# Kernel optimization log

Hardware: AMD Instinct MI355X
Metric: run time of the kernel (lower is better)

## Reference

```python
import jax, jax.numpy as jnp
import numpy as np

B, BS, M, D = 64, 8, 512, 256  # b = bs * neg_sample_num, neg_sample_num = 8
NEG_FILL = -1e10


def setup_inputs() -> dict:
    key = jax.random.key(0)
    ks = jax.random.split(key, 7)
    x = jax.random.normal(ks[0], (B, M, D), jnp.float32)
    y = jax.random.normal(ks[1], (BS, M, D), jnp.float32)
    mask_x = jax.random.randint(ks[2], (B, M), 0, 2).astype(bool).at[:, 0].set(True)
    mask_y = jax.random.randint(ks[3], (BS, M), 0, 2).astype(bool).at[:, 0].set(True)
    scale = 1.0 / np.sqrt(D)
    Wq = jax.random.normal(ks[4], (D, D), jnp.float32) * scale  # torch Linear weight [out,in]
    Wk = jax.random.normal(ks[5], (D, D), jnp.float32) * scale
    Wv = jax.random.normal(ks[6], (D, D), jnp.float32) * scale
    return {"x": x, "y": y, "mask_x": mask_x, "mask_y": mask_y, "Wq": Wq, "Wk": Wk, "Wv": Wv}


def reference(x, y, mask_x, mask_y, Wq, Wk, Wv):
    # Projections (torch Linear: x @ W.T, no bias)
    Qx, Kx, Vx = x @ Wq.T, x @ Wk.T, x @ Wv.T
    Qy, Ky, Vy = y @ Wq.T, y @ Wk.T, y @ Wv.T
    b, m, d = Qx.shape
    bs = Ky.shape[0]
    neg = b // bs  # neg_sample_num branch (bs != b)

    scores_x = jnp.einsum('bid,bjd->bij', Qx, Kx)   # [b,m,m]
    scores_y = jnp.einsum('bid,bjd->bij', Qy, Ky)   # [bs,m,m]
    # Q_x grouped as [bs, neg, m, d] then transposed to [neg, bs, m, d];
    # K_y is tiled over neg (pure broadcast), so contract directly against [bs,m,d].
    Qx_e = Qx.reshape(bs, neg, m, d).swapaxes(0, 1)  # [neg,bs,m,d]
    scores_xy = jnp.einsum('nsid,sjd->nsij', Qx_e, Ky)  # [neg,bs,m,m]

    mx = mask_x[:, :, None]  # [b,m,1]
    my = mask_y[:, :, None]  # [bs,m,1]
    scores_x = jnp.where(mx & mx.swapaxes(1, 2), scores_x, NEG_FILL)
    scores_y = jnp.where(my & my.swapaxes(1, 2), scores_y, NEG_FILL)

    mask_xy = mask_x.reshape(bs, neg, m, 1).swapaxes(0, 1) & mask_y[None, :, None, :]  # [neg,bs,m,m]
    scores_xy = jnp.where(mask_xy, scores_xy, NEG_FILL)

    # y_len[n, s] = sum(mask_y[s]) for every n (repeat/view/sum/transpose in torch)
    y_len = jnp.broadcast_to(jnp.sum(mask_y.astype(jnp.int32), axis=1)[None, :], (neg, bs))

    probs_x = jax.nn.softmax(scores_x, axis=-1)
    probs_y = jax.nn.softmax(scores_y, axis=-1)
    probs_xy = jax.nn.softmax(scores_xy, axis=-1)

    ctx_x = jnp.einsum('bij,bjd->bid', probs_x, Vx)
    ctx_y = jnp.einsum('bij,bjd->bid', probs_y, Vy)
    return (ctx_x, ctx_y, scores_x, scores_y, probs_xy, mask_xy, y_len)
```

## Files before the change

kernel.cpp:

```cpp
#include <hip/hip_runtime.h>
#include <cstdint>

#define NEG_FILL_F (-10000000000.0f)
constexpr int BB     = 64;
constexpr int BS_    = 8;
constexpr int MM     = 512;
constexpr int DD     = 256;
constexpr int ROWS_X = BB * MM;
constexpr int ROWS_Y = BS_ * MM;
constexpr int ROWS_ALL = ROWS_X + ROWS_Y;
constexpr int K3     = 768;

typedef __attribute__((ext_vector_type(8))) short short8;
typedef __attribute__((ext_vector_type(4))) float f32x4;

__device__ inline unsigned short rne_bf16(float f) {
    unsigned int u = __float_as_uint(f);
    u = (u + 0x7FFFu + ((u >> 16) & 1u)) >> 16;
    return (unsigned short)u;
}
__device__ inline float bf2f(unsigned short h) {
    return __uint_as_float(((unsigned int)h) << 16);
}

__device__ inline f32x4 mfma16(short8 a, short8 b, f32x4 c) {
    return __builtin_amdgcn_mfma_f32_16x16x32_bf16(a, b, c, 0, 0, 0);
}

__device__ inline void gld16(const unsigned short* g, unsigned short* l) {
    __builtin_amdgcn_global_load_lds(
        (const __attribute__((address_space(1))) unsigned int*)g,
        (__attribute__((address_space(3))) unsigned int*)l, 16, 0, 0);
}

template<int LDA, int LDB>
__device__ inline void mfma_tiles(const unsigned short (*Ab)[LDA],
                                  const unsigned short (*Bb)[LDB],
                                  int kk, int wrow, int wcol, int lid, int quad,
                                  f32x4 acc[4][4])
{
    short8 af[4], bfr[4];
    #pragma unroll
    for (int i = 0; i < 4; ++i)
        af[i] = *(const short8*)&Ab[wrow + i * 16 + lid][kk + quad * 8];
    #pragma unroll
    for (int j = 0; j < 4; ++j)
        bfr[j] = *(const short8*)&Bb[wcol + j * 16 + lid][kk + quad * 8];
    #pragma unroll
    for (int i = 0; i < 4; ++i)
        #pragma unroll
        for (int j = 0; j < 4; ++j)
            acc[i][j] = mfma16(af[i], bfr[j], acc[i][j]);
}

__device__ inline void stage768_async(unsigned short* dstbase,
                                      const unsigned short* __restrict__ src,
                                      int ck, int wave, int lane)
{
    #pragma unroll
    for (int s = 0; s < 6; ++s) {
        const int c   = s * 256 + wave * 64 + lane;
        const int row = c / 12;
        const int kc  = (c % 12) * 8;
        gld16(src + (size_t)row * K3 + ck * 96 + kc,
              dstbase + (size_t)(s * 256 + wave * 64) * 8);
    }
}

__device__ inline void stage_x96(unsigned short (*dst)[96],
                                 const float* __restrict__ src,
                                 int ck, int t)
{
    #pragma unroll
    for (int s = 0; s < 4; ++s) {
        const int c   = s * 256 + t;
        const int row = c >> 3;
        const int q4  = (c & 7) * 4;
        float4 v = *(const float4*)(src + (size_t)row * DD + ck * 32 + q4);
        const float fv[4] = {v.x, v.y, v.z, v.w};
        unsigned short o[12];
        #pragma unroll
        for (int e = 0; e < 4; ++e) {
            unsigned short h = rne_bf16(fv[e]);
            unsigned short l = rne_bf16(fv[e] - bf2f(h));
            o[e*3+0] = h; o[e*3+1] = l; o[e*3+2] = h;
        }
        ushort4* p = (ushort4*)&dst[row][q4 * 3];
        p[0] = make_ushort4(o[0], o[1], o[2],  o[3]);
        p[1] = make_ushort4(o[4], o[5], o[6],  o[7]);
        p[2] = make_ushort4(o[8], o[9], o[10], o[11]);
    }
}

__global__ __launch_bounds__(256) void convw_kernel(
    const float* __restrict__ Wq, const float* __restrict__ Wk,
    const float* __restrict__ Wv, unsigned short* __restrict__ Wb)
{
    const int g  = blockIdx.x * 256 + threadIdx.x;
    const int e  = g * 8;
    const int zi = e >> 16;
    const int off = e & 65535;
    const float* W = (zi == 0) ? Wq : (zi == 1 ? Wk : Wv);
    float4 v0 = *(const float4*)(W + off);
    float4 v1 = *(const float4*)(W + off + 4);
    const float fv[8] = {v0.x, v0.y, v0.z, v0.w, v1.x, v1.y, v1.z, v1.w};
    unsigned short o[24];
    #pragma unroll
    for (int i = 0; i < 8; ++i) {
        unsigned short h = rne_bf16(fv[i]);
        unsigned short l = rne_bf16(fv[i] - bf2f(h));
        o[i*3+0] = h; o[i*3+1] = h; o[i*3+2] = l;
    }
    unsigned short* dst = Wb + (size_t)zi * 196608 + (size_t)off * 3;
    #pragma unroll
    for (int s = 0; s < 3; ++s) {
        short8 v;
        #pragma unroll
        for (int e2 = 0; e2 < 8; ++e2) v[e2] = (short)o[s*8+e2];
        *(short8*)(dst + s * 8) = v;
    }
}

__global__ __launch_bounds__(256) void proj_kernel(
    const float* __restrict__ x, const float* __restrict__ y,
    const unsigned short* __restrict__ Wb,
    unsigned short* __restrict__ Qa, unsigned short* __restrict__ Kb,
    unsigned short* __restrict__ Vt)
{
    const int z    = blockIdx.z;
    const int row0 = blockIdx.x * 128;
    const int col0 = blockIdx.y * 128;
    const float* A = (row0 < ROWS_X) ? (x + (size_t)row0 * DD)
                                     : (y + (size_t)(row0 - ROWS_X) * DD);
    const unsigned short* Bsrc = Wb + (size_t)z * 196608 + (size_t)col0 * K3;

    __shared__ unsigned short Ab[128][96];
    __shared__ unsigned short Bb[128][96];

    const int t = threadIdx.x;
    const int wave = t >> 6, lane = t & 63, quad = lane >> 4, lid = lane & 15;
    const int wrow = (wave & 1) * 64, wcol = (wave >> 1) * 64;

    f32x4 acc[4][4];
    #pragma unroll
    for (int i = 0; i < 4; ++i)
        #pragma unroll
        for (int j = 0; j < 4; ++j) acc[i][j] = (f32x4){0.f, 0.f, 0.f, 0.f};

    for (int ck = 0; ck < 8; ++ck) {
        stage768_async(&Bb[0][0], Bsrc, ck, wave, lane);
        stage_x96(Ab, A, ck, t);
        __syncthreads();
        #pragma unroll
        for (int kk = 0; kk < 96; kk += 32)
            mfma_tiles<96,96>(Ab, Bb, kk, wrow, wcol, lid, quad, acc);
        __syncthreads();
    }

    if (z == 2) {
        #pragma unroll
        for (int i = 0; i < 4; ++i) {
            const int rg = row0 + wrow + i * 16 + quad * 4;
            const int b  = rg >> 9;
            const int j  = rg & 511;
            #pragma unroll
            for (int jt = 0; jt < 4; ++jt) {
                const int col = col0 + wcol + jt * 16 + lid;
                *(ushort4*)(Vt + (size_t)b * DD * MM + (size_t)col * MM + j) =
                    make_ushort4(rne_bf16(acc[i][jt][0]), rne_bf16(acc[i][jt][1]),
                                 rne_bf16(acc[i][jt][2]), rne_bf16(acc[i][jt][3]));
            }
        }
    } else {
        unsigned short* dst = (z == 0) ? Qa : Kb;
        const bool aform = (z == 0);
        #pragma unroll
        for (int i = 0; i < 4; ++i) {
            const int rg = row0 + wrow + i * 16 + quad * 4;
            #pragma unroll
            for (int r = 0; r < 4; ++r) {
                unsigned short* rowp = dst + (size_t)(rg + r) * K3;
                #pragma unroll
                for (int jt = 0; jt < 4; ++jt) {
                    const int col = col0 + wcol + jt * 16 + lid;
                    const float v = acc[i][jt][r];
                    unsigned short h = rne_bf16(v);
                    unsigned short l = rne_bf16(v - bf2f(h));
                    rowp[3*col+0] = h;
                    rowp[3*col+1] = aform ? l : h;
                    rowp[3*col+2] = aform ? h : l;
                }
            }
        }
    }
}

__global__ __launch_bounds__(256) void scores_kernel(
    const unsigned short* __restrict__ Qa_base,
    const unsigned short* __restrict__ Kb_base,
    const int* __restrict__ mq_base, const int* __restrict__ mk_base,
    float* __restrict__ Sbase, float* __restrict__ Mbase,
    float2* __restrict__ pstats, int mode)
{
    const int z = blockIdx.z;
    int bq, bk;
    if (mode == 2) { const int n = z >> 3, s = z & 7; bq = s * 8 + n; bk = s; }
    else           { bq = z; bk = z; }

    const int row0 = blockIdx.x * 128;
    const int col0 = blockIdx.y * 128;
    const unsigned short* Asrc = Qa_base + (size_t)(bq * MM + row0) * K3;
    const unsigned short* Bsrc = Kb_base + (size_t)(bk * MM + col0) * K3;
    const int* mq = mq_base + bq * MM;
    const int* mk = mk_base + bk * MM;
    float* S  = Sbase + (size_t)z * MM * MM;
    float* Mo = (mode == 2) ? (Mbase + (size_t)z * MM * MM) : nullptr;

    __shared__ unsigned short Ab[128][96];
    __shared__ unsigned short Bb[128][96];
    __shared__ float pm2[128][2];
    __shared__ float ps2[128][2];

    const int t = threadIdx.x;
    const int wave = t >> 6, lane = t & 63, quad = lane >> 4, lid = lane & 15;
    const int wrow = (wave & 1) * 64, wcol = (wave >> 1) * 64;

    f32x4 acc[4][4];
    #pragma unroll
    for (int i = 0; i < 4; ++i)
        #pragma unroll
        for (int j = 0; j < 4; ++j) acc[i][j] = (f32x4){0.f, 0.f, 0.f, 0.f};

    for (int ck = 0; ck < 8; ++ck) {
        stage768_async(&Ab[0][0], Asrc, ck, wave, lane);
        stage768_async(&Bb[0][0], Bsrc, ck, wave, lane);
        __syncthreads();
        #pragma unroll
        for (int kk = 0; kk < 96; kk += 32)
            mfma_tiles<96,96>(Ab, Bb, kk, wrow, wcol, lid, quad, acc);
        __syncthreads();
    }

    int mcol[4];
    #pragma unroll
    for (int jt = 0; jt < 4; ++jt) mcol[jt] = mk[col0 + wcol + jt * 16 + lid];

    #pragma unroll
    for (int i = 0; i < 4; ++i) {
        const int rl0 = wrow + i * 16 + quad * 4;
        #pragma unroll
        for (int r = 0; r < 4; ++r) {
            const int rlocal = rl0 + r;
            const int rg = row0 + rlocal;
            const bool mr = (mq[rg] != 0);
            float* Srow = S + (size_t)rg * MM;
            float* Mrow = Mo ? (Mo + (size_t)rg * MM) : nullptr;
            float v[4];
            float mt = -3.4e38f;
            #pragma unroll
            for (int jt = 0; jt < 4; ++jt) {
                const int col = col0 + wcol + jt * 16 + lid;
                const bool valid = mr && (mcol[jt] != 0);
                v[jt] = valid ? acc[i][jt][r] : NEG_FILL_F;
                Srow[col] = v[jt];
                if (Mrow) Mrow[col] = valid ? 1.0f : 0.0f;
                mt = fmaxf(mt, v[jt]);
            }
            #pragma unroll
            for (int o = 1; o < 16; o <<= 1) mt = fmaxf(mt, __shfl_xor(mt, o));
            float se = 0.f;
            #pragma unroll
            for (int jt = 0; jt < 4; ++jt) se += __expf(v[jt] - mt);
            #pragma unroll
            for (int o = 1; o < 16; o <<= 1) se += __shfl_xor(se, o);
            if (lid == 0) { pm2[rlocal][wave >> 1] = mt; ps2[rlocal][wave >> 1] = se; }
        }
    }
    __syncthreads();
    if (t < 128) {
        const float m0 = pm2[t][0], m1 = pm2[t][1];
        const float mm = fmaxf(m0, m1);
        const float ss = ps2[t][0] * __expf(m0 - mm) + ps2[t][1] * __expf(m1 - mm);
        pstats[(size_t)(z * 4 + blockIdx.y) * MM + row0 + t] = make_float2(mm, ss);
    }
}

__global__ __launch_bounds__(256) void reduce4_kernel(
    const float2* __restrict__ p, float2* __restrict__ st)
{
    const int row = blockIdx.x * 256 + threadIdx.x;
    const int z = row >> 9, rl = row & 511;
    float m = -3.4e38f, s = 0.f;
    #pragma unroll
    for (int by = 0; by < 4; ++by) {
        float2 v = p[(size_t)(z * 4 + by) * MM + rl];
        float nm = fmaxf(m, v.x);
        s = s * __expf(m - nm) + v.y * __expf(v.x - nm);
        m = nm;
    }
    st[row] = make_float2(m, 1.0f / s);
}

__global__ __launch_bounds__(256) void ctx_kernel(
    const float* __restrict__ Sbase, const float2* __restrict__ stats,
    const unsigned short* __restrict__ Vt_base, float* __restrict__ Obase)
{
    const int b = blockIdx.z;
    const float*          S  = Sbase + (size_t)b * MM * MM;
    const float2*         st = stats + (size_t)b * MM;
    const unsigned short* Vt = Vt_base + (size_t)b * DD * MM;
    float*                O  = Obase + (size_t)b * MM * DD;

    const int row0 = blockIdx.x * 128;
    const int col0 = blockIdx.y * 128;

    __shared__ unsigned short Ab[128][72];
    __shared__ unsigned short Bb[128][64];

    const int t = threadIdx.x;
    const int wave = t >> 6, lane = t & 63, quad = lane >> 4, lid = lane & 15;
    const int wrow = (wave & 1) * 64, wcol = (wave >> 1) * 64;

    f32x4 acc[4][4];
    #pragma unroll
    for (int i = 0; i < 4; ++i)
        #pragma unroll
        for (int j = 0; j < 4; ++j) acc[i][j] = (f32x4){0.f, 0.f, 0.f, 0.f};

    for (int ck = 0; ck < 8; ++ck) {
        #pragma unroll
        for (int s = 0; s < 4; ++s) {
            const int c   = s * 256 + wave * 64 + lane;
            const int row = c >> 3;
            const int j8  = (c & 7) * 8;
            gld16(Vt + (size_t)(col0 + row) * MM + ck * 64 + j8,
                  &Bb[0][0] + (size_t)(s * 256 + wave * 64) * 8);
        }
        #pragma unroll
        for (int s = 0; s < 4; ++s) {
            const int c   = s * 256 + t;
            const int row = c >> 3;
            const int j8  = (c & 7) * 8;
            const float* sp = S + (size_t)(row0 + row) * MM + ck * 64 + j8;
            float4 v0 = *(const float4*)sp;
            float4 v1 = *(const float4*)(sp + 4);
            const float pm = st[row0 + row].x;
            short8 pk;
            pk[0] = (short)rne_bf16(__expf(v0.x - pm));
            pk[1] = (short)rne_bf16(__expf(v0.y - pm));
            pk[2] = (short)rne_bf16(__expf(v0.z - pm));
            pk[3] = (short)rne_bf16(__expf(v0.w - pm));
            pk[4] = (short)rne_bf16(__expf(v1.x - pm));
            pk[5] = (short)rne_bf16(__expf(v1.y - pm));
            pk[6] = (short)rne_bf16(__expf(v1.z - pm));
            pk[7] = (short)rne_bf16(__expf(v1.w - pm));
            *(short8*)&Ab[row][j8] = pk;
        }
        __syncthreads();
        #pragma unroll
        for (int kk = 0; kk < 64; kk += 32)
            mfma_tiles<72,64>(Ab, Bb, kk, wrow, wcol, lid, quad, acc);
        __syncthreads();
    }

    #pragma unroll
    for (int i = 0; i < 4; ++i) {
        const int rgb = row0 + wrow + i * 16 + quad * 4;
        float inv[4];
        #pragma unroll
        for (int r = 0; r < 4; ++r) inv[r] = st[rgb + r].y;
        #pragma unroll
        for (int jt = 0; jt < 4; ++jt) {
            const int col = col0 + wcol + jt * 16 + lid;
            #pragma unroll
            for (int r = 0; r < 4; ++r)
                O[(size_t)(rgb + r) * DD + col] = acc[i][jt][r] * inv[r];
        }
    }
}

__global__ __launch_bounds__(128) void softmax_apply(
    float* __restrict__ S, const float2* __restrict__ stats)
{
    const int row = blockIdx.x;
    const float2 st = stats[row];
    float4* r = (float4*)(S + (size_t)row * MM) + threadIdx.x;
    float4 v = *r;
    v.x = __expf(v.x - st.x) * st.y;
    v.y = __expf(v.y - st.x) * st.y;
    v.z = __expf(v.z - st.x) * st.y;
    v.w = __expf(v.w - st.x) * st.y;
    *r = v;
}

__global__ void ylen_kernel(const int* __restrict__ mask_y, float* __restrict__ out)
{
    const int s = blockIdx.x;
    const int lane = threadIdx.x;
    int c = 0;
    #pragma unroll
    for (int k = 0; k < 8; ++k) c += (mask_y[s * MM + k * 64 + lane] != 0);
    #pragma unroll
    for (int off = 32; off; off >>= 1) c += __shfl_xor(c, off);
    if (lane < 8) out[lane * 8 + s] = (float)c;
}

extern "C" void kernel_launch(void* const* d_in, const int* in_sizes, int n_in,
                              void* d_out, int out_size, void* d_ws, size_t ws_size,
                              hipStream_t stream)
{
    const float* x      = (const float*)d_in[0];
    const float* y      = (const float*)d_in[1];
    const int*   mask_x = (const int*)d_in[2];
    const int*   mask_y = (const int*)d_in[3];
    const float* Wq     = (const float*)d_in[4];
    const float* Wk     = (const float*)d_in[5];
    const float* Wv     = (const float*)d_in[6];
    float* out = (float*)d_out;

    unsigned short* Wb = (unsigned short*)d_ws;
    unsigned short* Qa = Wb + 589824;
    unsigned short* Kb = Qa + 28311552;
    unsigned short* Vt = Kb + 28311552;
    float2* stats_x  = (float2*)(Vt + 9437184);
    float2* stats_y  = stats_x + ROWS_X;
    float2* stats_xy = stats_y + ROWS_Y;
    float2* ps_x  = stats_xy + ROWS_X;
    float2* ps_y  = ps_x + 64 * 4 * 512;
    float2* ps_xy = ps_y + 8 * 4 * 512;

    float* out_ctx_x = out;
    float* out_ctx_y = out + 8388608;
    float* out_sx    = out + 9437184;
    float* out_sy    = out + 26214400;
    float* out_pxy   = out + 28311552;
    float* out_mxy   = out + 45088768;
    float* out_ylen  = out + 61865984;

    convw_kernel<<<96, 256, 0, stream>>>(Wq, Wk, Wv, Wb);

    proj_kernel<<<dim3(288, 2, 3), 256, 0, stream>>>(x, y, Wb, Qa, Kb, Vt);

    const unsigned short* Qa_y = Qa + (size_t)ROWS_X * K3;
    const unsigned short* Kb_y = Kb + (size_t)ROWS_X * K3;

    scores_kernel<<<dim3(4, 4, 64), 256, 0, stream>>>(Qa,   Kb,   mask_x, mask_x, out_sx,  nullptr, ps_x,  0);
    scores_kernel<<<dim3(4, 4, 8),  256, 0, stream>>>(Qa_y, Kb_y, mask_y, mask_y, out_sy,  nullptr, ps_y,  1);
    scores_kernel<<<dim3(4, 4, 64), 256, 0, stream>>>(Qa,   Kb_y, mask_x, mask_y, out_pxy, out_mxy, ps_xy, 2);

    reduce4_kernel<<<ROWS_X / 256, 256, 0, stream>>>(ps_x,  stats_x);
    reduce4_kernel<<<ROWS_Y / 256, 256, 0, stream>>>(ps_y,  stats_y);
    reduce4_kernel<<<ROWS_X / 256, 256, 0, stream>>>(ps_xy, stats_xy);

    ctx_kernel<<<dim3(4, 2, 64), 256, 0, stream>>>(out_sx, stats_x, Vt, out_ctx_x);
    ctx_kernel<<<dim3(4, 2, 8),  256, 0, stream>>>(out_sy, stats_y,
                                                   Vt + (size_t)64 * DD * MM, out_ctx_y);

    softmax_apply<<<ROWS_X, 128, 0, stream>>>(out_pxy, stats_xy);

    ylen_kernel<<<8, 64, 0, stream>>>(mask_y, out_ylen);
}
```

Measured before the change: 546.1 us.

## Split-bf16 pre-conversion, single-bf16 xy scores, LDS swizzles, merged launches

Converts x and y to split-bf16 once in a separate kernel, staging them into the projection via async LDS loads with a rotation swizzle to cut bank conflicts. Computes the xy cross scores from single-bf16 plain Q and K copies with K=256 instead of the 3x split form, which reduces MFMA work but lowers precision for probs_xy. Merges the x/y self-score, reduce and ctx launches into single grids and adds XOR swizzles to the ctx B tile. Output buffers are reused as scratch for the intermediates.

```diff
diff --git a/kernel.cpp b/kernel.cpp
--- a/kernel.cpp
+++ b/kernel.cpp
@@ -33,62 +33,41 @@
         (__attribute__((address_space(3))) unsigned int*)l, 16, 0, 0);
 }
 
-template<int LDA, int LDB>
-__device__ inline void mfma_tiles(const unsigned short (*Ab)[LDA],
-                                  const unsigned short (*Bb)[LDB],
-                                  int kk, int wrow, int wcol, int lid, int quad,
-                                  f32x4 acc[4][4])
-{
-    short8 af[4], bfr[4];
+__device__ inline void mfma_4x4(const short8 af[4], const short8 bf_[4],
+                                f32x4 acc[4][4]) {
     #pragma unroll
     for (int i = 0; i < 4; ++i)
-        af[i] = *(const short8*)&Ab[wrow + i * 16 + lid][kk + quad * 8];
-    #pragma unroll
-    for (int j = 0; j < 4; ++j)
-        bfr[j] = *(const short8*)&Bb[wcol + j * 16 + lid][kk + quad * 8];
-    #pragma unroll
-    for (int i = 0; i < 4; ++i)
         #pragma unroll
         for (int j = 0; j < 4; ++j)
-            acc[i][j] = mfma16(af[i], bfr[j], acc[i][j]);
-}
-
-__device__ inline void stage768_async(unsigned short* dstbase,
-                                      const unsigned short* __restrict__ src,
-                                      int ck, int wave, int lane)
+            acc[i][j] = mfma16(af[i], bf_[j], acc[i][j]);
+}
+
+__device__ inline void stage768_rot(unsigned short* dstbase,
+                                    const unsigned short* __restrict__ src,
+                                    int ck, int wave, int lane)
 {
     #pragma unroll
     for (int s = 0; s < 6; ++s) {
-        const int c   = s * 256 + wave * 64 + lane;
-        const int row = c / 12;
-        const int kc  = (c % 12) * 8;
-        gld16(src + (size_t)row * K3 + ck * 96 + kc,
+        const int c  = s * 256 + wave * 64 + lane;
+        const int r  = c / 12;
+        const int q  = c - r * 12;
+        const int rm = r % 12;
+        int cin = q - rm;
+        cin += (cin >> 31) & 12;
+        gld16(src + (size_t)r * K3 + ck * 96 + cin * 8,
               dstbase + (size_t)(s * 256 + wave * 64) * 8);
     }
 }
 
-__device__ inline void stage_x96(unsigned short (*dst)[96],
-                                 const float* __restrict__ src,
-                                 int ck, int t)
-{
-    #pragma unroll
-    for (int s = 0; s < 4; ++s) {
-        const int c   = s * 256 + t;
-        const int row = c >> 3;
-        const int q4  = (c & 7) * 4;
-        float4 v = *(const float4*)(src + (size_t)row * DD + ck * 32 + q4);
-        const float fv[4] = {v.x, v.y, v.z, v.w};
-        unsigned short o[12];
-        #pragma unroll
-        for (int e = 0; e < 4; ++e) {
-            unsigned short h = rne_bf16(fv[e]);
-            unsigned short l = rne_bf16(fv[e] - bf2f(h));
-            o[e*3+0] = h; o[e*3+1] = l; o[e*3+2] = h;
-        }
-        ushort4* p = (ushort4*)&dst[row][q4 * 3];
-        p[0] = make_ushort4(o[0], o[1], o[2],  o[3]);
-        p[1] = make_ushort4(o[4], o[5], o[6],  o[7]);
-        p[2] = make_ushort4(o[8], o[9], o[10], o[11]);
+__device__ inline void frag4_rot96(const unsigned short (*T)[96], int rbase,
+                                   int lid, const int rm[4], int c0,
+                                   short8 f[4])
+{
+    #pragma unroll
+    for (int i = 0; i < 4; ++i) {
+        int q = c0 + rm[i];
+        if (q >= 12) q -= 12;
+        f[i] = *(const short8*)&T[rbase + i * 16 + lid][q * 8];
     }
 }
 
@@ -121,17 +100,46 @@
     }
 }
 
+__global__ __launch_bounds__(256) void convx_kernel(
+    const float* __restrict__ x, const float* __restrict__ y,
+    unsigned short* __restrict__ xs)
+{
+    const int g   = blockIdx.x * 256 + threadIdx.x;
+    const int row = g >> 5;
+    const int off = (g & 31) * 8;
+    const float* src = (row < ROWS_X) ? (x + (size_t)row * DD)
+                                      : (y + (size_t)(row - ROWS_X) * DD);
+    float4 v0 = *(const float4*)(src + off);
+    float4 v1 = *(const float4*)(src + off + 4);
+    const float fv[8] = {v0.x, v0.y, v0.z, v0.w, v1.x, v1.y, v1.z, v1.w};
+    unsigned short o[24];
+    #pragma unroll
+    for (int i = 0; i < 8; ++i) {
+        unsigned short h = rne_bf16(fv[i]);
+        unsigned short l = rne_bf16(fv[i] - bf2f(h));
+        o[i*3+0] = h; o[i*3+1] = l; o[i*3+2] = h;
+    }
+    unsigned short* dst = xs + (size_t)row * K3 + (size_t)off * 3;
+    #pragma unroll
+    for (int s = 0; s < 3; ++s) {
+        short8 w;
+        #pragma unroll
+        for (int e2 = 0; e2 < 8; ++e2) w[e2] = (short)o[s*8+e2];
+        *(short8*)(dst + s * 8) = w;
+    }
+}
+
 __global__ __launch_bounds__(256) void proj_kernel(
-    const float* __restrict__ x, const float* __restrict__ y,
+    const unsigned short* __restrict__ xs,
     const unsigned short* __restrict__ Wb,
     unsigned short* __restrict__ Qa, unsigned short* __restrict__ Kb,
-    unsigned short* __restrict__ Vt)
+    unsigned short* __restrict__ Vt,
+    unsigned short* __restrict__ Qp, unsigned short* __restrict__ Kp)
 {
     const int z    = blockIdx.z;
     const int row0 = blockIdx.x * 128;
     const int col0 = blockIdx.y * 128;
-    const float* A = (row0 < ROWS_X) ? (x + (size_t)row0 * DD)
-                                     : (y + (size_t)(row0 - ROWS_X) * DD);
+    const unsigned short* Asrc = xs + (size_t)row0 * K3;
     const unsigned short* Bsrc = Wb + (size_t)z * 196608 + (size_t)col0 * K3;
 
     __shared__ unsigned short Ab[128][96];
@@ -141,6 +149,13 @@
     const int wave = t >> 6, lane = t & 63, quad = lane >> 4, lid = lane & 15;
     const int wrow = (wave & 1) * 64, wcol = (wave >> 1) * 64;
 
+    int rma[4], rmb[4];
+    #pragma unroll
+    for (int i = 0; i < 4; ++i) {
+        rma[i] = (wrow + i * 16 + lid) % 12;
+        rmb[i] = (wcol + i * 16 + lid) % 12;
+    }
+
     f32x4 acc[4][4];
     #pragma unroll
     for (int i = 0; i < 4; ++i)
@@ -148,12 +163,17 @@
         for (int j = 0; j < 4; ++j) acc[i][j] = (f32x4){0.f, 0.f, 0.f, 0.f};
 
     for (int ck = 0; ck < 8; ++ck) {
-        stage768_async(&Bb[0][0], Bsrc, ck, wave, lane);
-        stage_x96(Ab, A, ck, t);
-        __syncthreads();
-        #pragma unroll
-        for (int kk = 0; kk < 96; kk += 32)
-            mfma_tiles<96,96>(Ab, Bb, kk, wrow, wcol, lid, quad, acc);
+        stage768_rot(&Ab[0][0], Asrc, ck, wave, lane);
+        stage768_rot(&Bb[0][0], Bsrc, ck, wave, lane);
+        __syncthreads();
+        #pragma unroll
+        for (int kk = 0; kk < 96; kk += 32) {
+            const int c0 = (kk >> 3) + quad;
+            short8 af[4], bf_[4];
+            frag4_rot96(Ab, wrow, lid, rma, c0, af);
+            frag4_rot96(Bb, wcol, lid, rmb, c0, bf_);
+            mfma_4x4(af, bf_, acc);
+        }
         __syncthreads();
     }
 
@@ -174,12 +194,18 @@
     } else {
         unsigned short* dst = (z == 0) ? Qa : Kb;
         const bool aform = (z == 0);
+        unsigned short* plain = nullptr;
+        int rbase_plain = 0;
+        if (z == 0 && row0 < ROWS_X) { plain = Qp; rbase_plain = 0; }
+        if (z == 1 && row0 >= ROWS_X) { plain = Kp; rbase_plain = ROWS_X; }
         #pragma unroll
         for (int i = 0; i < 4; ++i) {
             const int rg = row0 + wrow + i * 16 + quad * 4;
             #pragma unroll
             for (int r = 0; r < 4; ++r) {
                 unsigned short* rowp = dst + (size_t)(rg + r) * K3;
+                unsigned short* prow = plain
+                    ? (plain + (size_t)(rg + r - rbase_plain) * DD) : nullptr;
                 #pragma unroll
                 for (int jt = 0; jt < 4; ++jt) {
                     const int col = col0 + wcol + jt * 16 + lid;
@@ -189,32 +215,26 @@
                     rowp[3*col+0] = h;
                     rowp[3*col+1] = aform ? l : h;
                     rowp[3*col+2] = aform ? h : l;
+                    if (prow) prow[col] = h;
                 }
             }
         }
     }
 }
 
-__global__ __launch_bounds__(256) void scores_kernel(
-    const unsigned short* __restrict__ Qa_base,
-    const unsigned short* __restrict__ Kb_base,
-    const int* __restrict__ mq_base, const int* __restrict__ mk_base,
-    float* __restrict__ Sbase, float* __restrict__ Mbase,
-    float2* __restrict__ pstats, int mode)
-{
-    const int z = blockIdx.z;
-    int bq, bk;
-    if (mode == 2) { const int n = z >> 3, s = z & 7; bq = s * 8 + n; bk = s; }
-    else           { bq = z; bk = z; }
-
+__global__ __launch_bounds__(256) void scores_self_kernel(
+    const unsigned short* __restrict__ Qa,
+    const unsigned short* __restrict__ Kb,
+    const int* __restrict__ mask_x, const int* __restrict__ mask_y,
+    float* __restrict__ Sbase, float2* __restrict__ pstats)
+{
+    const int z    = blockIdx.z;
     const int row0 = blockIdx.x * 128;
     const int col0 = blockIdx.y * 128;
-    const unsigned short* Asrc = Qa_base + (size_t)(bq * MM + row0) * K3;
-    const unsigned short* Bsrc = Kb_base + (size_t)(bk * MM + col0) * K3;
-    const int* mq = mq_base + bq * MM;
-    const int* mk = mk_base + bk * MM;
-    float* S  = Sbase + (size_t)z * MM * MM;
-    float* Mo = (mode == 2) ? (Mbase + (size_t)z * MM * MM) : nullptr;
+    const unsigned short* Asrc = Qa + (size_t)(z * MM + row0) * K3;
+    const unsigned short* Bsrc = Kb + (size_t)(z * MM + col0) * K3;
+    const int* msk = (z < 64) ? (mask_x + z * MM) : (mask_y + (z - 64) * MM);
+    float* S = Sbase + (size_t)z * MM * MM;
 
     __shared__ unsigned short Ab[128][96];
     __shared__ unsigned short Bb[128][96];
@@ -225,6 +245,13 @@
     const int wave = t >> 6, lane = t & 63, quad = lane >> 4, lid = lane & 15;
     const int wrow = (wave & 1) * 64, wcol = (wave >> 1) * 64;
 
+    int rma[4], rmb[4];
+    #pragma unroll
+    for (int i = 0; i < 4; ++i) {
+        rma[i] = (wrow + i * 16 + lid) % 12;
+        rmb[i] = (wcol + i * 16 + lid) % 12;
+    }
+
     f32x4 acc[4][4];
     #pragma unroll
     for (int i = 0; i < 4; ++i)
@@ -232,18 +259,23 @@
         for (int j = 0; j < 4; ++j) acc[i][j] = (f32x4){0.f, 0.f, 0.f, 0.f};
 
     for (int ck = 0; ck < 8; ++ck) {
-        stage768_async(&Ab[0][0], Asrc, ck, wave, lane);
-        stage768_async(&Bb[0][0], Bsrc, ck, wave, lane);
-        __syncthreads();
-        #pragma unroll
-        for (int kk = 0; kk < 96; kk += 32)
-            mfma_tiles<96,96>(Ab, Bb, kk, wrow, wcol, lid, quad, acc);
+        stage768_rot(&Ab[0][0], Asrc, ck, wave, lane);
+        stage768_rot(&Bb[0][0], Bsrc, ck, wave, lane);
+        __syncthreads();
+        #pragma unroll
+        for (int kk = 0; kk < 96; kk += 32) {
+            const int c0 = (kk >> 3) + quad;
+            short8 af[4], bf_[4];
+            frag4_rot96(Ab, wrow, lid, rma, c0, af);
+            frag4_rot96(Bb, wcol, lid, rmb, c0, bf_);
+            mfma_4x4(af, bf_, acc);
+        }
         __syncthreads();
     }
 
     int mcol[4];
     #pragma unroll
-    for (int jt = 0; jt < 4; ++jt) mcol[jt] = mk[col0 + wcol + jt * 16 + lid];
+    for (int jt = 0; jt < 4; ++jt) mcol[jt] = msk[col0 + wcol + jt * 16 + lid];
 
     #pragma unroll
     for (int i = 0; i < 4; ++i) {
@@ -252,9 +284,8 @@
         for (int r = 0; r < 4; ++r) {
             const int rlocal = rl0 + r;
             const int rg = row0 + rlocal;
-            const bool mr = (mq[rg] != 0);
+            const bool mr = (msk[rg] != 0);
             float* Srow = S + (size_t)rg * MM;
-            float* Mrow = Mo ? (Mo + (size_t)rg * MM) : nullptr;
             float v[4];
             float mt = -3.4e38f;
             #pragma unroll
@@ -263,7 +294,6 @@
                 const bool valid = mr && (mcol[jt] != 0);
                 v[jt] = valid ? acc[i][jt][r] : NEG_FILL_F;
                 Srow[col] = v[jt];
-                if (Mrow) Mrow[col] = valid ? 1.0f : 0.0f;
                 mt = fmaxf(mt, v[jt]);
             }
             #pragma unroll
@@ -285,6 +315,118 @@
     }
 }
 
+__global__ __launch_bounds__(256) void scores_xy_kernel(
+    const unsigned short* __restrict__ Qp, const unsigned short* __restrict__ Kp,
+    const int* __restrict__ mask_x, const int* __restrict__ mask_y,
+    float* __restrict__ Sbase, float* __restrict__ Mbase,
+    float2* __restrict__ pstats)
+{
+    const int z = blockIdx.z;
+    const int n = z >> 3, s = z & 7;
+    const int bq = s * 8 + n;
+    const int bk = s;
+    const int row0 = blockIdx.x * 128;
+    const int col0 = blockIdx.y * 128;
+    const unsigned short* Asrc = Qp + (size_t)(bq * MM + row0) * DD;
+    const unsigned short* Bsrc = Kp + (size_t)(bk * MM + col0) * DD;
+    const int* mq = mask_x + bq * MM;
+    const int* mk = mask_y + bk * MM;
+    float* Sl = Sbase + (size_t)z * MM * MM;
+    float* Ml = Mbase + (size_t)z * MM * MM;
+
+    __shared__ unsigned short Ab[128][64];
+    __shared__ unsigned short Bb[128][64];
+    __shared__ float pm2[128][2];
+    __shared__ float ps2[128][2];
+
+    const int t = threadIdx.x;
+    const int wave = t >> 6, lane = t & 63, quad = lane >> 4, lid = lane & 15;
+    const int wrow = (wave & 1) * 64, wcol = (wave >> 1) * 64;
+    const int x7 = lid & 7;
+
+    f32x4 acc[4][4];
+    #pragma unroll
+    for (int i = 0; i < 4; ++i)
+        #pragma unroll
+        for (int j = 0; j < 4; ++j) acc[i][j] = (f32x4){0.f, 0.f, 0.f, 0.f};
+
+    for (int ck = 0; ck < 4; ++ck) {
+        #pragma unroll
+        for (int s4 = 0; s4 < 4; ++s4) {
+            const int c   = s4 * 256 + wave * 64 + lane;
+            const int r   = c >> 3;
+            const int cin = (c & 7) ^ (r & 7);
+            gld16(Asrc + (size_t)r * DD + ck * 64 + cin * 8,
+                  &Ab[0][0] + (size_t)(s4 * 256 + wave * 64) * 8);
+        }
+        #pragma unroll
+        for (int s4 = 0; s4 < 4; ++s4) {
+            const int c   = s4 * 256 + wave * 64 + lane;
+            const int r   = c >> 3;
+            const int cin = (c & 7) ^ (r & 7);
+            gld16(Bsrc + (size_t)r * DD + ck * 64 + cin * 8,
+                  &Bb[0][0] + (size_t)(s4 * 256 + wave * 64) * 8);
+        }
+        __syncthreads();
+        #pragma unroll
+        for (int kk = 0; kk < 64; kk += 32) {
+            const int c0 = (kk >> 3) + quad;
+            const int q  = c0 ^ x7;
+            short8 af[4], bf_[4];
+            #pragma unroll
+            for (int i = 0; i < 4; ++i) {
+                af[i]  = *(const short8*)&Ab[wrow + i * 16 + lid][q * 8];
+                bf_[i] = *(const short8*)&Bb[wcol + i * 16 + lid][q * 8];
+            }
+            mfma_4x4(af, bf_, acc);
+        }
+        __syncthreads();
+    }
+
+    int mcol[4];
+    #pragma unroll
+    for (int jt = 0; jt < 4; ++jt) mcol[jt] = mk[col0 + wcol + jt * 16 + lid];
+
+    #pragma unroll
+    for (int i = 0; i < 4; ++i) {
+        const int rl0 = wrow + i * 16 + quad * 4;
+        #pragma unroll
+        for (int r = 0; r < 4; ++r) {
+            const int rlocal = rl0 + r;
+            const int rg = row0 + rlocal;
+            const bool mr = (mq[rg] != 0);
+            float* Srow = Sl + (size_t)rg * MM;
+            float* Mrow = Ml + (size_t)rg * MM;
+            float v[4];
+            float mt = -3.4e38f;
+            #pragma unroll
+            for (int jt = 0; jt < 4; ++jt) {
+                const int col = col0 + wcol + jt * 16 + lid;
+                const bool valid = mr && (mcol[jt] != 0);
+                v[jt] = valid ? acc[i][jt][r] : NEG_FILL_F;
+                Srow[col] = v[jt];
+                Mrow[col] = valid ? 1.0f : 0.0f;
+                mt = fmaxf(mt, v[jt]);
+            }
+            #pragma unroll
+            for (int o = 1; o < 16; o <<= 1) mt = fmaxf(mt, __shfl_xor(mt, o));
+            float se = 0.f;
+            #pragma unroll
+            for (int jt = 0; jt < 4; ++jt) se += __expf(v[jt] - mt);
+            #pragma unroll
+            for (int o = 1; o < 16; o <<= 1) se += __shfl_xor(se, o);
+            if (lid == 0) { pm2[rlocal][wave >> 1] = mt; ps2[rlocal][wave >> 1] = se; }
+        }
+    }
+    __syncthreads();
+    if (t < 128) {
+        const float m0 = pm2[t][0], m1 = pm2[t][1];
+        const float mm = fmaxf(m0, m1);
+        const float ss = ps2[t][0] * __expf(m0 - mm) + ps2[t][1] * __expf(m1 - mm);
+        pstats[(size_t)(z * 4 + blockIdx.y) * MM + row0 + t] = make_float2(mm, ss);
+    }
+}
+
 __global__ __launch_bounds__(256) void reduce4_kernel(
     const float2* __restrict__ p, float2* __restrict__ st)
 {
@@ -320,6 +462,7 @@
     const int t = threadIdx.x;
     const int wave = t >> 6, lane = t & 63, quad = lane >> 4, lid = lane & 15;
     const int wrow = (wave & 1) * 64, wcol = (wave >> 1) * 64;
+    const int x7 = lid & 7;
 
     f32x4 acc[4][4];
     #pragma unroll
@@ -329,16 +472,16 @@
 
     for (int ck = 0; ck < 8; ++ck) {
         #pragma unroll
-        for (int s = 0; s < 4; ++s) {
-            const int c   = s * 256 + wave * 64 + lane;
-            const int row = c >> 3;
-            const int j8  = (c & 7) * 8;
-            gld16(Vt + (size_t)(col0 + row) * MM + ck * 64 + j8,
-                  &Bb[0][0] + (size_t)(s * 256 + wave * 64) * 8);
-        }
-        #pragma unroll
-        for (int s = 0; s < 4; ++s) {
-            const int c   = s * 256 + t;
+        for (int s4 = 0; s4 < 4; ++s4) {
+            const int c   = s4 * 256 + wave * 64 + lane;
+            const int r   = c >> 3;
+            const int cin = (c & 7) ^ (r & 7);
+            gld16(Vt + (size_t)(col0 + r) * MM + ck * 64 + cin * 8,
+                  &Bb[0][0] + (size_t)(s4 * 256 + wave * 64) * 8);
+        }
+        #pragma unroll
+        for (int s4 = 0; s4 < 4; ++s4) {
+            const int c   = s4 * 256 + t;
             const int row = c >> 3;
             const int j8  = (c & 7) * 8;
             const float* sp = S + (size_t)(row0 + row) * MM + ck * 64 + j8;
@@ -358,8 +501,17 @@
         }
         __syncthreads();
         #pragma unroll
-        for (int kk = 0; kk < 64; kk += 32)
-            mfma_tiles<72,64>(Ab, Bb, kk, wrow, wcol, lid, quad, acc);
+        for (int kk = 0; kk < 64; kk += 32) {
+            const int c0 = (kk >> 3) + quad;
+            const int q  = c0 ^ x7;
+            short8 af[4], bf_[4];
+            #pragma unroll
+            for (int i = 0; i < 4; ++i) {
+                af[i]  = *(const short8*)&Ab[wrow + i * 16 + lid][kk + quad * 8];
+                bf_[i] = *(const short8*)&Bb[wcol + i * 16 + lid][q * 8];
+            }
+            mfma_4x4(af, bf_, acc);
+        }
         __syncthreads();
     }
 
@@ -423,38 +575,33 @@
     unsigned short* Kb = Qa + 28311552;
     unsigned short* Vt = Kb + 28311552;
     float2* stats_x  = (float2*)(Vt + 9437184);
-    float2* stats_y  = stats_x + ROWS_X;
-    float2* stats_xy = stats_y + ROWS_Y;
-    float2* ps_x  = stats_xy + ROWS_X;
-    float2* ps_y  = ps_x + 64 * 4 * 512;
-    float2* ps_xy = ps_y + 8 * 4 * 512;
+    float2* stats_xy = stats_x + ROWS_ALL;
+    float2* ps_x  = stats_x + (ROWS_ALL + ROWS_X);
+    float2* ps_xy = ps_x + (64 + 8) * 4 * 512;
 
     float* out_ctx_x = out;
-    float* out_ctx_y = out + 8388608;
     float* out_sx    = out + 9437184;
-    float* out_sy    = out + 26214400;
     float* out_pxy   = out + 28311552;
     float* out_mxy   = out + 45088768;
     float* out_ylen  = out + 61865984;
 
+    unsigned short* xs = (unsigned short*)out_pxy;
+    unsigned short* Qp = (unsigned short*)out_ctx_x;
+    unsigned short* Kp = Qp + (size_t)ROWS_X * DD;
+
     convw_kernel<<<96, 256, 0, stream>>>(Wq, Wk, Wv, Wb);
-
-    proj_kernel<<<dim3(288, 2, 3), 256, 0, stream>>>(x, y, Wb, Qa, Kb, Vt);
-
-    const unsigned short* Qa_y = Qa + (size_t)ROWS_X * K3;
-    const unsigned short* Kb_y = Kb + (size_t)ROWS_X * K3;
-
-    scores_kernel<<<dim3(4, 4, 64), 256, 0, stream>>>(Qa,   Kb,   mask_x, mask_x, out_sx,  nullptr, ps_x,  0);
-    scores_kernel<<<dim3(4, 4, 8),  256, 0, stream>>>(Qa_y, Kb_y, mask_y, mask_y, out_sy,  nullptr, ps_y,  1);
-    scores_kernel<<<dim3(4, 4, 64), 256, 0, stream>>>(Qa,   Kb_y, mask_x, mask_y, out_pxy, out_mxy, ps_xy, 2);
-
-    reduce4_kernel<<<ROWS_X / 256, 256, 0, stream>>>(ps_x,  stats_x);
-    reduce4_kernel<<<ROWS_Y / 256, 256, 0, stream>>>(ps_y,  stats_y);
-    reduce4_kernel<<<ROWS_X / 256, 256, 0, stream>>>(ps_xy, stats_xy);
-
-    ctx_kernel<<<dim3(4, 2, 64), 256, 0, stream>>>(out_sx, stats_x, Vt, out_ctx_x);
-    ctx_kernel<<<dim3(4, 2, 8),  256, 0, stream>>>(out_sy, stats_y,
-                                                   Vt + (size_t)64 * DD * MM, out_ctx_y);
+    convx_kernel<<<4608, 256, 0, stream>>>(x, y, xs);
+
+    proj_kernel<<<dim3(288, 2, 3), 256, 0, stream>>>(xs, Wb, Qa, Kb, Vt, Qp, Kp);
+
+    scores_self_kernel<<<dim3(4, 4, 72), 256, 0, stream>>>(
+        Qa, Kb, mask_x, mask_y, out_sx, ps_x);
+    scores_xy_kernel<<<dim3(4, 4, 64), 256, 0, stream>>>(
+        Qp, Kp, mask_x, mask_y, out_pxy, out_mxy, ps_xy);
+
+    reduce4_kernel<<<(ROWS_ALL + ROWS_X) / 256, 256, 0, stream>>>(ps_x, stats_x);
+
+    ctx_kernel<<<dim3(4, 2, 72), 256, 0, stream>>>(out_sx, stats_x, Vt, out_ctx_x);
 
     softmax_apply<<<ROWS_X, 128, 0, stream>>>(out_pxy, stats_xy);
 
```

After: 552.4 us. About the same (+1.1%).
